# Performance work log

Hardware: AMD Instinct MI355X
Metric: run time of the kernel (lower is better)

Reference implementation:

```python
import jax, jax.numpy as jnp
import numpy as np

FEATS = 1024
HEAD = 16
DH = FEATS // HEAD
B, N = 2, 2048
SQRT_D = FEATS ** 0.5  # note: source scales by sqrt(feats), not sqrt(head_dim)


def setup_inputs() -> dict:
    key = jax.random.key(0)
    ks = jax.random.split(key, 9)
    s = 1.0 / np.sqrt(FEATS)
    return {
        "x": jax.random.normal(ks[0], (B, N, FEATS), dtype=jnp.float32),
        "Wq": jax.random.normal(ks[1], (FEATS, FEATS), dtype=jnp.float32) * s,
        "bq": jax.random.normal(ks[2], (FEATS,), dtype=jnp.float32) * s,
        "Wk": jax.random.normal(ks[3], (FEATS, FEATS), dtype=jnp.float32) * s,
        "bk": jax.random.normal(ks[4], (FEATS,), dtype=jnp.float32) * s,
        "Wv": jax.random.normal(ks[5], (FEATS, FEATS), dtype=jnp.float32) * s,
        "bv": jax.random.normal(ks[6], (FEATS,), dtype=jnp.float32) * s,
        "Wo": jax.random.normal(ks[7], (FEATS, FEATS), dtype=jnp.float32) * s,
        "bo": jax.random.normal(ks[8], (FEATS,), dtype=jnp.float32) * s,
    }


def reference(x, Wq, bq, Wk, bk, Wv, bv, Wo, bo):
    b, n, f = x.shape
    # Linear layers: y = x @ W^T + b (torch nn.Linear convention)
    q = (x @ Wq.T + bq).reshape(b, n, HEAD, DH).transpose(0, 2, 1, 3)  # bhnd
    k = (x @ Wk.T + bk).reshape(b, n, HEAD, DH).transpose(0, 2, 1, 3)
    v = (x @ Wv.T + bv).reshape(b, n, HEAD, DH).transpose(0, 2, 1, 3)
    score = jax.nn.softmax(jnp.einsum('bhif,bhjf->bhij', q, k) / SQRT_D, axis=-1)
    attn = jnp.einsum('bhij,bhjf->bihf', score, v)  # [b, n, head, dh]
    o = attn.reshape(b, n, f) @ Wo.T + bo
    return o
```

## Files before the change

kernel.cpp:

```cpp
#include <hip/hip_runtime.h>
#include <stdint.h>

typedef short short8 __attribute__((ext_vector_type(8)));
typedef float f32x4 __attribute__((ext_vector_type(4)));
typedef float f32x16 __attribute__((ext_vector_type(16)));
typedef unsigned int uint2v __attribute__((ext_vector_type(2)));
typedef unsigned int uint4v __attribute__((ext_vector_type(4)));

#define SEQ 2048
#define NBH 32

__device__ __forceinline__ unsigned short f32_to_bf16(float f) {
  union { float f; uint32_t u; } v; v.f = f;
  return (unsigned short)((v.u + 0x7fffu + ((v.u >> 16) & 1u)) >> 16);
}

__device__ __forceinline__ float bf16_to_f32(unsigned short u) {
  union { uint32_t u; float f; } v; v.u = ((uint32_t)u) << 16;
  return v.f;
}

__device__ __forceinline__ unsigned int cvtpk_bf16(float lo, float hi) {
  unsigned int r;
  asm("v_cvt_pk_bf16_f32 %0, %1, %2" : "=v"(r) : "v"(lo), "v"(hi));
  return r;
}

__device__ __forceinline__ void gload_lds16(const unsigned short* g, unsigned short* l) {
  __builtin_amdgcn_global_load_lds(
      (const __attribute__((address_space(1))) unsigned int*)g,
      (__attribute__((address_space(3))) unsigned int*)l, 16, 0, 0);
}

__global__ void cast_all(const float* __restrict__ x,
                         const float* __restrict__ Wq, const float* __restrict__ Wk,
                         const float* __restrict__ Wv, const float* __restrict__ Wo,
                         unsigned short* __restrict__ ws0) {
  int g = blockIdx.x * blockDim.x + threadIdx.x;
  int wi = g >> 18, gl = g & 262143;
  const float* src; int off;
  if (wi < 4)      { src = x;  off = g;  }
  else if (wi == 4){ src = Wq; off = gl; }
  else if (wi == 5){ src = Wk; off = gl; }
  else if (wi == 6){ src = Wv; off = gl; }
  else             { src = Wo; off = gl; }
  float4 v = ((const float4*)src)[off];
  ushort4 o;
  o.x = f32_to_bf16(v.x); o.y = f32_to_bf16(v.y);
  o.z = f32_to_bf16(v.z); o.w = f32_to_bf16(v.w);
  ((ushort4*)ws0)[g] = o;
}

#define GSWZ(row, k) ((k) ^ ((row) & 3) ^ (((row) >> 2) & 3))

__device__ __forceinline__ void gemm_core_1024(
    const unsigned short* __restrict__ Ag,
    const unsigned short* __restrict__ Bg,
    int tid, f32x4 acc[4][4])
{
  __shared__ __align__(16) unsigned short As[128 * 32];
  __shared__ __align__(16) unsigned short Bs[128 * 32];
  const int w = tid >> 6, l = tid & 63;
  const int wr = w >> 1, wc = w & 1;
  const int lc = l & 15, lg = l >> 4;

  const int c0row = tid >> 2,        c0ks = tid & 3;
  const int c1row = (256 + tid) >> 2;

  for (int k0 = 0; k0 < 1024; k0 += 32) {
    int kg0 = GSWZ(c0row, c0ks);
    int kg1 = GSWZ(c1row, c0ks);
    gload_lds16(Ag + (size_t)c0row * 1024 + k0 + kg0 * 8, As + (w * 64) * 8);
    gload_lds16(Ag + (size_t)c1row * 1024 + k0 + kg1 * 8, As + (256 + w * 64) * 8);
    gload_lds16(Bg + (size_t)c0row * 1024 + k0 + kg0 * 8, Bs + (w * 64) * 8);
    gload_lds16(Bg + (size_t)c1row * 1024 + k0 + kg1 * 8, Bs + (256 + w * 64) * 8);
    __syncthreads();

    short8 a[4], b[4];
#pragma unroll
    for (int mi = 0; mi < 4; ++mi) {
      int row = wr * 64 + mi * 16 + lc;
      int ko = GSWZ(row, lg);
      a[mi] = *(const short8*)(As + row * 32 + ko * 8);
    }
#pragma unroll
    for (int ni = 0; ni < 4; ++ni) {
      int row = wc * 64 + ni * 16 + lc;
      int ko = GSWZ(row, lg);
      b[ni] = *(const short8*)(Bs + row * 32 + ko * 8);
    }
#pragma unroll
    for (int mi = 0; mi < 4; ++mi)
#pragma unroll
      for (int ni = 0; ni < 4; ++ni)
        acc[mi][ni] = __builtin_amdgcn_mfma_f32_16x16x32_bf16(a[mi], b[ni], acc[mi][ni], 0, 0, 0);
    __syncthreads();
  }
}

__global__ __launch_bounds__(256, 3)
void gemm_qkv(const unsigned short* __restrict__ XB,
              const unsigned short* __restrict__ WQB,
              const unsigned short* __restrict__ WKB,
              const unsigned short* __restrict__ WVB,
              const float* __restrict__ bq,
              const float* __restrict__ bk,
              const float* __restrict__ bv,
              unsigned short* __restrict__ Qo,
              unsigned short* __restrict__ Ko,
              unsigned short* __restrict__ VTo)
{
  const int tid = threadIdx.x;
  const int tm = blockIdx.x * 128;
  const int tn = blockIdx.y * 128;
  const int wi = tn >> 10;
  const int tnl = tn & 1023;
  const unsigned short* Bw = (wi == 0 ? WQB : wi == 1 ? WKB : WVB) + (size_t)tnl * 1024;
  const float* bias = (wi == 0 ? bq : wi == 1 ? bk : bv);
  const float qscale = (wi == 0) ? 0.04508422002778011f : 1.0f;

  f32x4 acc[4][4];
#pragma unroll
  for (int mi = 0; mi < 4; ++mi)
#pragma unroll
    for (int ni = 0; ni < 4; ++ni)
      acc[mi][ni] = (f32x4){0.f, 0.f, 0.f, 0.f};

  gemm_core_1024(XB + (size_t)tm * 1024, Bw, tid, acc);

  const int w = tid >> 6, l = tid & 63;
  const int wr = w >> 1, wc = w & 1;
  const int lc = l & 15, lg = l >> 4;

  if (wi == 2) {
#pragma unroll
    for (int ni = 0; ni < 4; ++ni) {
      int nl = tnl + wc * 64 + ni * 16 + lc;
      float bb = bias[nl];
      int h = nl >> 6, d = nl & 63;
#pragma unroll
      for (int mi = 0; mi < 4; ++mi) {
        int ibase = tm + wr * 64 + mi * 16 + lg * 4;
        int b = ibase >> 11, i = ibase & 2047;
        uint2v pk;
        pk.x = cvtpk_bf16(acc[mi][ni][0] + bb, acc[mi][ni][1] + bb);
        pk.y = cvtpk_bf16(acc[mi][ni][2] + bb, acc[mi][ni][3] + bb);
        *(uint2v*)(VTo + (((size_t)(b * 16 + h) * 64 + d) * SEQ + i)) = pk;
      }
    }
  } else {
    unsigned short* Out = (wi == 0) ? Qo : Ko;
#pragma unroll
    for (int ni = 0; ni < 4; ++ni) {
      int nl = tnl + wc * 64 + ni * 16 + lc;
      float bb = bias[nl];
      int h = nl >> 6, d = nl & 63;
#pragma unroll
      for (int mi = 0; mi < 4; ++mi) {
#pragma unroll
        for (int r = 0; r < 4; ++r) {
          int m = tm + wr * 64 + mi * 16 + lg * 4 + r;
          int b = m >> 11, i = m & 2047;
          float v = (acc[mi][ni][r] + bb) * qscale;
          Out[(((size_t)(b * 16 + h) * SEQ + i) << 6) + d] = f32_to_bf16(v);
        }
      }
    }
  }
}

__global__ __launch_bounds__(256, 2)
void gemm_o(const unsigned short* __restrict__ AT,
            const unsigned short* __restrict__ WOB,
            const float* __restrict__ bo,
            float* __restrict__ Of)
{
  __shared__ __align__(16) unsigned short As[64 * 32];
  __shared__ __align__(16) unsigned short Bs[128 * 32];
  const int tid = threadIdx.x;
  const int w = tid >> 6, l = tid & 63;
  const int lc = l & 15, lg = l >> 4;
  const int tm = blockIdx.x * 64;
  const int tn = blockIdx.y * 128;
  const unsigned short* Ag = AT + (size_t)tm * 1024;
  const unsigned short* Bg = WOB + (size_t)tn * 1024;

  const int crow = tid >> 2, cks = tid & 3;

  f32x4 acc[4][2];
#pragma unroll
  for (int mi = 0; mi < 4; ++mi)
#pragma unroll
    for (int ni = 0; ni < 2; ++ni)
      acc[mi][ni] = (f32x4){0.f, 0.f, 0.f, 0.f};

  for (int k0 = 0; k0 < 1024; k0 += 32) {
    int kg = GSWZ(crow, cks);
    gload_lds16(Ag + (size_t)crow * 1024 + k0 + kg * 8, As + w * 512);
    gload_lds16(Bg + (size_t)crow * 1024 + k0 + kg * 8, Bs + w * 512);
    gload_lds16(Bg + (size_t)(64 + crow) * 1024 + k0 + kg * 8, Bs + 2048 + w * 512);
    __syncthreads();

    short8 a[4], b[2];
#pragma unroll
    for (int mi = 0; mi < 4; ++mi) {
      int row = mi * 16 + lc;
      a[mi] = *(const short8*)(As + row * 32 + GSWZ(row, lg) * 8);
    }
#pragma unroll
    for (int ni = 0; ni < 2; ++ni) {
      int row = w * 32 + ni * 16 + lc;
      b[ni] = *(const short8*)(Bs + row * 32 + GSWZ(row, lg) * 8);
    }
#pragma unroll
    for (int mi = 0; mi < 4; ++mi)
#pragma unroll
      for (int ni = 0; ni < 2; ++ni)
        acc[mi][ni] = __builtin_amdgcn_mfma_f32_16x16x32_bf16(a[mi], b[ni], acc[mi][ni], 0, 0, 0);
    __syncthreads();
  }

#pragma unroll
  for (int ni = 0; ni < 2; ++ni) {
    int n = tn + w * 32 + ni * 16 + lc;
    float bb = bo[n];
#pragma unroll
    for (int mi = 0; mi < 4; ++mi) {
#pragma unroll
      for (int r = 0; r < 4; ++r) {
        int m = tm + mi * 16 + lg * 4 + r;
        Of[(size_t)m * 1024 + n] = acc[mi][ni][r] + bb;
      }
    }
  }
}

__global__ __launch_bounds__(256, 4)
void attn_fwd7(const unsigned short* __restrict__ Qm,
               const unsigned short* __restrict__ Km,
               const unsigned short* __restrict__ VTm,
               unsigned short* __restrict__ Op0,
               unsigned short* __restrict__ Op1,
               float* __restrict__ Lp)
{
  __shared__ __align__(16) unsigned short KV[2][64 * 128];
  const int tid = threadIdx.x, w = tid >> 6, l = tid & 63;
  const int lq = l & 31, hi = l >> 5;
  const int m15 = lq & 15;
  const int bh = blockIdx.x, q0 = blockIdx.y * 128;
  const int js = blockIdx.z;
  const int j0 = js << 10;

  const unsigned short* Qb = Qm + ((size_t)bh * SEQ + q0 + w * 32) * 64;
  const unsigned short* Kg = Km + ((size_t)bh * SEQ + j0) * 64;
  const unsigned short* Vg = VTm + (size_t)bh * 64 * SEQ + j0;

  const int sr = l >> 4;
  const int ss = l & 15;
  const unsigned short* sp[4];
  int sstep[4];
#pragma unroll
  for (int i = 0; i < 4; ++i) {
    int r = w * 16 + i * 4 + sr;
    int t = ss ^ (i * 4 + sr);
    if (t < 8) { sp[i] = Kg + (size_t)r * 64 + t * 8;          sstep[i] = 64 * 64; }
    else       { sp[i] = Vg + (size_t)r * SEQ + (t - 8) * 8;   sstep[i] = 64; }
  }

  short8 qf[4];
#pragma unroll
  for (int kc = 0; kc < 4; ++kc)
    qf[kc] = *(const short8*)(Qb + lq * 64 + kc * 16 + hi * 8);

  f32x16 o0, o1;
#pragma unroll
  for (int r = 0; r < 16; ++r) { o0[r] = 0.f; o1[r] = 0.f; }
  float sm[8];
#pragma unroll
  for (int i = 0; i < 8; ++i) sm[i] = 0.f;

#pragma unroll
  for (int i = 0; i < 4; ++i) {
    gload_lds16(sp[i], &KV[0][(w * 16 + i * 4) * 128]);
    sp[i] += sstep[i];
  }
  __syncthreads();

  for (int t = 0; t < 16; ++t) {
    const int cur = t & 1;
    if (t + 1 < 16) {
#pragma unroll
      for (int i = 0; i < 4; ++i) {
        gload_lds16(sp[i], &KV[cur ^ 1][(w * 16 + i * 4) * 128]);
        sp[i] += sstep[i];
      }
    }
    const char* Tb = (const char*)(&KV[cur][0]);

    f32x16 s0, s1;
#pragma unroll
    for (int r = 0; r < 16; ++r) { s0[r] = 0.f; s1[r] = 0.f; }
    __builtin_amdgcn_s_setprio(1);
#pragma unroll
    for (int kc = 0; kc < 4; ++kc) {
      short8 kf = *(const short8*)(Tb + lq * 256 + (((kc * 2 + hi) ^ m15) << 4));
      s0 = __builtin_amdgcn_mfma_f32_32x32x16_bf16(kf, qf[kc], s0, 0, 0, 0);
    }
#pragma unroll
    for (int kc = 0; kc < 4; ++kc) {
      short8 kf = *(const short8*)(Tb + (32 + lq) * 256 + (((kc * 2 + hi) ^ m15) << 4));
      s1 = __builtin_amdgcn_mfma_f32_32x32x16_bf16(kf, qf[kc], s1, 0, 0, 0);
    }
    __builtin_amdgcn_s_setprio(0);

    float p[32];
#pragma unroll
    for (int r = 0; r < 16; ++r) {
      p[r] = __builtin_amdgcn_exp2f(s0[r]);
      p[16 + r] = __builtin_amdgcn_exp2f(s1[r]);
    }
#pragma unroll
    for (int i = 0; i < 8; ++i)
      sm[i] += (p[i] + p[i + 8]) + (p[i + 16] + p[i + 24]);

    short8 pa[4];
#pragma unroll
    for (int ks = 0; ks < 4; ++ks) {
      const int pb = ks * 8;
      unsigned int a0 = cvtpk_bf16(p[pb + 0], p[pb + 1]);
      unsigned int a1 = cvtpk_bf16(p[pb + 2], p[pb + 3]);
      unsigned int b0 = cvtpk_bf16(p[pb + 4], p[pb + 5]);
      unsigned int b1 = cvtpk_bf16(p[pb + 6], p[pb + 7]);
      unsigned int a0x = __shfl_xor((int)a0, 32), b0x = __shfl_xor((int)b0, 32);
      unsigned int a1x = __shfl_xor((int)a1, 32), b1x = __shfl_xor((int)b1, 32);
      union { uint4v u; short8 s; } cvt;
      cvt.u.x = hi ? b0x : a0;
      cvt.u.y = hi ? b1x : a1;
      cvt.u.z = hi ? b0 : a0x;
      cvt.u.w = hi ? b1 : a1x;
      pa[ks] = cvt.s;
    }

    __builtin_amdgcn_s_setprio(1);
#pragma unroll
    for (int ks = 0; ks < 4; ++ks) {
      short8 vf = *(const short8*)(Tb + lq * 256 + (((8 + ks * 2 + hi) ^ m15) << 4));
      o0 = __builtin_amdgcn_mfma_f32_32x32x16_bf16(vf, pa[ks], o0, 0, 0, 0);
    }
#pragma unroll
    for (int ks = 0; ks < 4; ++ks) {
      short8 vf = *(const short8*)(Tb + (32 + lq) * 256 + (((8 + ks * 2 + hi) ^ m15) << 4));
      o1 = __builtin_amdgcn_mfma_f32_32x32x16_bf16(vf, pa[ks], o1, 0, 0, 0);
    }
    __builtin_amdgcn_s_setprio(0);
    __syncthreads();
  }

  float lden = ((sm[0] + sm[1]) + (sm[2] + sm[3])) + ((sm[4] + sm[5]) + (sm[6] + sm[7]));
  lden += __shfl_xor(lden, 32);
  const int b = bh >> 4, h = bh & 15;
  const int iq = q0 + w * 32 + lq;
  unsigned short* Op = js ? Op1 : Op0;
  if (hi == 0) Lp[(size_t)js * (NBH * SEQ) + (size_t)bh * SEQ + iq] = lden;
  const size_t obase = ((size_t)b * SEQ + iq) * 1024 + h * 64;
#pragma unroll
  for (int rq = 0; rq < 4; ++rq) {
    uint2v pk0, pk1;
    pk0.x = cvtpk_bf16(o0[rq * 4 + 0], o0[rq * 4 + 1]);
    pk0.y = cvtpk_bf16(o0[rq * 4 + 2], o0[rq * 4 + 3]);
    pk1.x = cvtpk_bf16(o1[rq * 4 + 0], o1[rq * 4 + 1]);
    pk1.y = cvtpk_bf16(o1[rq * 4 + 2], o1[rq * 4 + 3]);
    *(uint2v*)(Op + obase + rq * 8 + hi * 4) = pk0;
    *(uint2v*)(Op + obase + 32 + rq * 8 + hi * 4) = pk1;
  }
}

__global__ __launch_bounds__(256)
void attn_norm(const unsigned short* __restrict__ Op0,
               const unsigned short* __restrict__ Op1,
               const float* __restrict__ Lp,
               unsigned short* __restrict__ ATB)
{
  const int b = blockIdx.y;
  const int g = blockIdx.x * 256 + threadIdx.x;
  const size_t gi = (size_t)b * 524288 + g;
  const ushort4 a = ((const ushort4*)Op0)[gi];
  const ushort4 c = ((const ushort4*)Op1)[gi];
  const int e = g << 2;
  const int i = e >> 10, col = e & 1023, h = col >> 6;
  const size_t lix = (size_t)((b << 4) + h) * SEQ + i;
  const float inv = 1.0f / (Lp[lix] + Lp[(size_t)NBH * SEQ + lix]);
  ushort4 o;
  o.x = f32_to_bf16((bf16_to_f32(a.x) + bf16_to_f32(c.x)) * inv);
  o.y = f32_to_bf16((bf16_to_f32(a.y) + bf16_to_f32(c.y)) * inv);
  o.z = f32_to_bf16((bf16_to_f32(a.z) + bf16_to_f32(c.z)) * inv);
  o.w = f32_to_bf16((bf16_to_f32(a.w) + bf16_to_f32(c.w)) * inv);
  ((ushort4*)ATB)[gi] = o;
}

extern "C" void kernel_launch(void* const* d_in, const int* in_sizes, int n_in,
                              void* d_out, int out_size, void* d_ws, size_t ws_size,
                              hipStream_t stream) {
  (void)in_sizes; (void)n_in; (void)out_size; (void)ws_size;
  const float* x  = (const float*)d_in[0];
  const float* Wq = (const float*)d_in[1];
  const float* bq = (const float*)d_in[2];
  const float* Wk = (const float*)d_in[3];
  const float* bk = (const float*)d_in[4];
  const float* Wv = (const float*)d_in[5];
  const float* bv = (const float*)d_in[6];
  const float* Wo = (const float*)d_in[7];
  const float* bo = (const float*)d_in[8];
  float* Of = (float*)d_out;

  unsigned short* ws  = (unsigned short*)d_ws;
  unsigned short* XB  = ws;
  unsigned short* WQB = ws + 4194304u;
  unsigned short* WKB = ws + 5242880u;
  unsigned short* WVB = ws + 6291456u;
  unsigned short* WOB = ws + 7340032u;
  unsigned short* QB  = ws + 8388608u;
  unsigned short* KB  = ws + 12582912u;
  unsigned short* VTB = ws + 20971520u;
  unsigned short* ATB = ws + 25165824u;
  unsigned short* Op0 = ws;
  unsigned short* Op1 = ws + 16777216u;
  float* Lp = (float*)(ws + 4194304u);

  cast_all<<<8192, 256, 0, stream>>>(x, Wq, Wk, Wv, Wo, ws);

  gemm_qkv<<<dim3(32, 24), 256, 0, stream>>>(XB, WQB, WKB, WVB, bq, bk, bv, QB, KB, VTB);

  attn_fwd7<<<dim3(32, 16, 2), 256, 0, stream>>>(QB, KB, VTB, Op0, Op1, Lp);
  attn_norm<<<dim3(2048, 2), 256, 0, stream>>>(Op0, Op1, Lp, ATB);
  gemm_o<<<dim3(64, 8), 256, 0, stream>>>(ATB, WOB, bo, Of);
}
```

Before: 119.2 us.

## Fuse split-softmax normalization into output GEMM and halve P-repack shuffles

Removes the separate attn_norm kernel: the output projection GEMM now loads both partial attention outputs, combines them and divides by the summed softmax denominators while staging its A tile into LDS. This drops a full intermediate bf16 write and re-read plus one launch. The A tile now goes through registers instead of direct-to-LDS loads, and each partial output is re-read by every column block, adding latency per k-step. Separately, the attention kernel's P-fragment repack selects values before shuffling so only two cross-lane shuffles are needed instead of four.

```diff
diff --git a/kernel.cpp b/kernel.cpp
--- a/kernel.cpp
+++ b/kernel.cpp
@@ -170,10 +170,12 @@
 }
 
 __global__ __launch_bounds__(256, 2)
-void gemm_o(const unsigned short* __restrict__ AT,
-            const unsigned short* __restrict__ WOB,
-            const float* __restrict__ bo,
-            float* __restrict__ Of)
+void gemm_o_norm(const unsigned short* __restrict__ Op0,
+                 const unsigned short* __restrict__ Op1,
+                 const float* __restrict__ Lp,
+                 const unsigned short* __restrict__ WOB,
+                 const float* __restrict__ bo,
+                 float* __restrict__ Of)
 {
   __shared__ __align__(16) unsigned short As[64 * 32];
   __shared__ __align__(16) unsigned short Bs[128 * 32];
@@ -182,10 +184,15 @@
   const int lc = l & 15, lg = l >> 4;
   const int tm = blockIdx.x * 64;
   const int tn = blockIdx.y * 128;
-  const unsigned short* Ag = AT + (size_t)tm * 1024;
   const unsigned short* Bg = WOB + (size_t)tn * 1024;
 
   const int crow = tid >> 2, cks = tid & 3;
+  const int m = tm + crow;
+  const int bb_ = m >> 11, ii = m & 2047;
+  const int kg = GSWZ(crow, cks);
+  const size_t abase = (size_t)m * 1024 + kg * 8;
+  const float* LpA = Lp + (size_t)(bb_ * 16) * SEQ + ii;
+  const float* LpB = LpA + (size_t)NBH * SEQ;
 
   f32x4 acc[4][2];
 #pragma unroll
@@ -195,10 +202,24 @@
       acc[mi][ni] = (f32x4){0.f, 0.f, 0.f, 0.f};
 
   for (int k0 = 0; k0 < 1024; k0 += 32) {
-    int kg = GSWZ(crow, cks);
-    gload_lds16(Ag + (size_t)crow * 1024 + k0 + kg * 8, As + w * 512);
     gload_lds16(Bg + (size_t)crow * 1024 + k0 + kg * 8, Bs + w * 512);
     gload_lds16(Bg + (size_t)(64 + crow) * 1024 + k0 + kg * 8, Bs + 2048 + w * 512);
+
+    const int h = k0 >> 6;
+    const float inv = 1.0f / (LpA[(size_t)h * SEQ] + LpB[(size_t)h * SEQ]);
+    union { uint4v v; unsigned short e[8]; } A0, A1;
+    A0.v = *(const uint4v*)(Op0 + abase + k0);
+    A1.v = *(const uint4v*)(Op1 + abase + k0);
+    uint4v wv;
+    wv.x = cvtpk_bf16((bf16_to_f32(A0.e[0]) + bf16_to_f32(A1.e[0])) * inv,
+                      (bf16_to_f32(A0.e[1]) + bf16_to_f32(A1.e[1])) * inv);
+    wv.y = cvtpk_bf16((bf16_to_f32(A0.e[2]) + bf16_to_f32(A1.e[2])) * inv,
+                      (bf16_to_f32(A0.e[3]) + bf16_to_f32(A1.e[3])) * inv);
+    wv.z = cvtpk_bf16((bf16_to_f32(A0.e[4]) + bf16_to_f32(A1.e[4])) * inv,
+                      (bf16_to_f32(A0.e[5]) + bf16_to_f32(A1.e[5])) * inv);
+    wv.w = cvtpk_bf16((bf16_to_f32(A0.e[6]) + bf16_to_f32(A1.e[6])) * inv,
+                      (bf16_to_f32(A0.e[7]) + bf16_to_f32(A1.e[7])) * inv);
+    *(uint4v*)(As + crow * 32 + cks * 8) = wv;
     __syncthreads();
 
     short8 a[4], b[2];
@@ -228,20 +249,20 @@
     for (int mi = 0; mi < 4; ++mi) {
 #pragma unroll
       for (int r = 0; r < 4; ++r) {
-        int m = tm + mi * 16 + lg * 4 + r;
-        Of[(size_t)m * 1024 + n] = acc[mi][ni][r] + bb;
+        int mm = tm + mi * 16 + lg * 4 + r;
+        Of[(size_t)mm * 1024 + n] = acc[mi][ni][r] + bb;
       }
     }
   }
 }
 
 __global__ __launch_bounds__(256, 4)
-void attn_fwd7(const unsigned short* __restrict__ Qm,
-               const unsigned short* __restrict__ Km,
-               const unsigned short* __restrict__ VTm,
-               unsigned short* __restrict__ Op0,
-               unsigned short* __restrict__ Op1,
-               float* __restrict__ Lp)
+void attn_fwd11(const unsigned short* __restrict__ Qm,
+                const unsigned short* __restrict__ Km,
+                const unsigned short* __restrict__ VTm,
+                unsigned short* __restrict__ Op0,
+                unsigned short* __restrict__ Op1,
+                float* __restrict__ Lp)
 {
   __shared__ __align__(16) unsigned short KV[2][64 * 128];
   const int tid = threadIdx.x, w = tid >> 6, l = tid & 63;
@@ -331,13 +352,15 @@
       unsigned int a1 = cvtpk_bf16(p[pb + 2], p[pb + 3]);
       unsigned int b0 = cvtpk_bf16(p[pb + 4], p[pb + 5]);
       unsigned int b1 = cvtpk_bf16(p[pb + 6], p[pb + 7]);
-      unsigned int a0x = __shfl_xor((int)a0, 32), b0x = __shfl_xor((int)b0, 32);
-      unsigned int a1x = __shfl_xor((int)a1, 32), b1x = __shfl_xor((int)b1, 32);
+      unsigned int s0v = hi ? a0 : b0;
+      unsigned int s1v = hi ? a1 : b1;
+      unsigned int r0 = __shfl_xor((int)s0v, 32);
+      unsigned int r1 = __shfl_xor((int)s1v, 32);
       union { uint4v u; short8 s; } cvt;
-      cvt.u.x = hi ? b0x : a0;
-      cvt.u.y = hi ? b1x : a1;
-      cvt.u.z = hi ? b0 : a0x;
-      cvt.u.w = hi ? b1 : a1x;
+      cvt.u.x = hi ? r0 : a0;
+      cvt.u.y = hi ? r1 : a1;
+      cvt.u.z = hi ? b0 : r0;
+      cvt.u.w = hi ? b1 : r1;
       pa[ks] = cvt.s;
     }
 
@@ -373,29 +396,6 @@
     *(uint2v*)(Op + obase + rq * 8 + hi * 4) = pk0;
     *(uint2v*)(Op + obase + 32 + rq * 8 + hi * 4) = pk1;
   }
-}
-
-__global__ __launch_bounds__(256)
-void attn_norm(const unsigned short* __restrict__ Op0,
-               const unsigned short* __restrict__ Op1,
-               const float* __restrict__ Lp,
-               unsigned short* __restrict__ ATB)
-{
-  const int b = blockIdx.y;
-  const int g = blockIdx.x * 256 + threadIdx.x;
-  const size_t gi = (size_t)b * 524288 + g;
-  const ushort4 a = ((const ushort4*)Op0)[gi];
-  const ushort4 c = ((const ushort4*)Op1)[gi];
-  const int e = g << 2;
-  const int i = e >> 10, col = e & 1023, h = col >> 6;
-  const size_t lix = (size_t)((b << 4) + h) * SEQ + i;
-  const float inv = 1.0f / (Lp[lix] + Lp[(size_t)NBH * SEQ + lix]);
-  ushort4 o;
-  o.x = f32_to_bf16((bf16_to_f32(a.x) + bf16_to_f32(c.x)) * inv);
-  o.y = f32_to_bf16((bf16_to_f32(a.y) + bf16_to_f32(c.y)) * inv);
-  o.z = f32_to_bf16((bf16_to_f32(a.z) + bf16_to_f32(c.z)) * inv);
-  o.w = f32_to_bf16((bf16_to_f32(a.w) + bf16_to_f32(c.w)) * inv);
-  ((ushort4*)ATB)[gi] = o;
 }
 
 extern "C" void kernel_launch(void* const* d_in, const int* in_sizes, int n_in,
@@ -422,7 +422,6 @@
   unsigned short* QB  = ws + 8388608u;
   unsigned short* KB  = ws + 12582912u;
   unsigned short* VTB = ws + 20971520u;
-  unsigned short* ATB = ws + 25165824u;
   unsigned short* Op0 = ws;
   unsigned short* Op1 = ws + 16777216u;
   float* Lp = (float*)(ws + 4194304u);
@@ -431,7 +430,6 @@
 
   gemm_qkv<<<dim3(32, 24), 256, 0, stream>>>(XB, WQB, WKB, WVB, bq, bk, bv, QB, KB, VTB);
 
-  attn_fwd7<<<dim3(32, 16, 2), 256, 0, stream>>>(QB, KB, VTB, Op0, Op1, Lp);
-  attn_norm<<<dim3(2048, 2), 256, 0, stream>>>(Op0, Op1, Lp, ATB);
-  gemm_o<<<dim3(64, 8), 256, 0, stream>>>(ATB, WOB, bo, Of);
-}
+  attn_fwd11<<<dim3(32, 16, 2), 256, 0, stream>>>(QB, KB, VTB, Op0, Op1, Lp);
+  gemm_o_norm<<<dim3(64, 8), 256, 0, stream>>>(Op0, Op1, Lp, WOB, bo, Of);
+}
```

Measured after the change: 117.2 us. Within noise of the previous version (-1.7%).
